# Optimization experiments

Hardware: AMD Instinct MI355X
Metric: run time of the kernel (lower is better)

Reference implementation:

```python
import jax, jax.numpy as jnp
import numpy as np

D_MODEL = 1024
NUM_HEADS = 16
D_K = D_MODEL // NUM_HEADS
D_MLP = 4096
EPS = 1e-5


def setup_inputs() -> dict:
    key = jax.random.key(0)
    ks = jax.random.split(key, 16)
    s = 0.02
    inp = {
        "x": jax.random.normal(ks[0], (2, 2048, D_MODEL), dtype=jnp.float32),
        "Wq": jax.random.normal(ks[1], (D_MODEL, D_MODEL), dtype=jnp.float32) * s,
        "bq": jnp.zeros((D_MODEL,), jnp.float32),
        "Wk": jax.random.normal(ks[2], (D_MODEL, D_MODEL), dtype=jnp.float32) * s,
        "bk": jnp.zeros((D_MODEL,), jnp.float32),
        "Wv": jax.random.normal(ks[3], (D_MODEL, D_MODEL), dtype=jnp.float32) * s,
        "bv": jnp.zeros((D_MODEL,), jnp.float32),
        "Wo": jax.random.normal(ks[4], (D_MODEL, D_MODEL), dtype=jnp.float32) * s,
        "bo": jnp.zeros((D_MODEL,), jnp.float32),
        "W1": jax.random.normal(ks[5], (D_MODEL, D_MLP), dtype=jnp.float32) * s,
        "b1": jnp.zeros((D_MLP,), jnp.float32),
        "W2": jax.random.normal(ks[6], (D_MLP, D_MODEL), dtype=jnp.float32) * s,
        "b2": jnp.zeros((D_MODEL,), jnp.float32),
        "ln1_g": jnp.ones((D_MODEL,), jnp.float32),
        "ln1_b": jnp.zeros((D_MODEL,), jnp.float32),
        "ln2_g": jnp.ones((D_MODEL,), jnp.float32),
        "ln2_b": jnp.zeros((D_MODEL,), jnp.float32),
    }
    return inp


def _layer_norm(x, g, b):
    mu = jnp.mean(x, axis=-1, keepdims=True)
    var = jnp.var(x, axis=-1, keepdims=True)
    return (x - mu) * jax.lax.rsqrt(var + EPS) * g + b


def _split_heads(x):
    b, s, _ = x.shape
    return x.reshape(b, s, NUM_HEADS, D_K).transpose(0, 2, 1, 3)  # [b,h,s,dk]


def reference(x, Wq, bq, Wk, bk, Wv, bv, Wo, bo, W1, b1, W2, b2,
              ln1_g, ln1_b, ln2_g, ln2_b):
    b, s, _ = x.shape
    q = _split_heads(x @ Wq + bq)
    k = _split_heads(x @ Wk + bk)
    v = _split_heads(x @ Wv + bv)
    # [b,h,s,s] scores, scaled by sqrt(d_k) as in the original
    score = jnp.einsum("bhqd,bhkd->bhqk", q, k) / jnp.sqrt(jnp.float32(D_K))
    attn = jax.nn.softmax(score, axis=-1)
    out = jnp.einsum("bhqk,bhkd->bhqd", attn, v)
    out = out.transpose(0, 2, 1, 3).reshape(b, s, D_MODEL)
    out = out @ Wo + bo
    # residual + norm1 (dropout is identity in eval)
    x = _layer_norm(x + out, ln1_g, ln1_b)
    # feed-forward
    h = jax.nn.relu(x @ W1 + b1)
    ff = h @ W2 + b2
    x = _layer_norm(x + ff, ln2_g, ln2_b)
    return x
```

## Files before the change

kernel.cpp:

```cpp
#include <hip/hip_runtime.h>
#include <hip/hip_bf16.h>
#include <cstdint>

#define DEV __device__ __forceinline__

typedef __attribute__((ext_vector_type(8))) __bf16 bf16x8;
typedef __attribute__((ext_vector_type(4))) float f32x4;

DEV uint16_t f2b(float f) {
  __hip_bfloat16 h = __float2bfloat16(f);
  return *(uint16_t*)&h;
}
DEV uint32_t pkbf2(float a, float b) {
  return (uint32_t)f2b(a) | ((uint32_t)f2b(b) << 16);
}

DEV void gload_lds16(const void* g, void* l) {
  __builtin_amdgcn_global_load_lds(
      (const __attribute__((address_space(1))) void*)g,
      (__attribute__((address_space(3))) void*)l, 16, 0, 0);
}

DEV bf16x8 scale8(bf16x8 v, float sc) {
  union { bf16x8 b; uint16_t u[8]; } in, out;
  in.b = v;
#pragma unroll
  for (int i = 0; i < 8; i++) {
    float x = __uint_as_float(((uint32_t)in.u[i]) << 16);
    out.u[i] = f2b(x * sc);
  }
  return out.b;
}

__global__ __launch_bounds__(256) void cast_bf16_kernel(
    const float* __restrict__ src, uint16_t* __restrict__ dst, int n4) {
  int i = blockIdx.x * 256 + threadIdx.x;
  if (i < n4) {
    float4 v = ((const float4*)src)[i];
    uint2 r;
    r.x = pkbf2(v.x, v.y);
    r.y = pkbf2(v.z, v.w);
    ((uint2*)dst)[i] = r;
  }
}

__global__ __launch_bounds__(256) void transpose_w(
    const float* __restrict__ src, uint16_t* __restrict__ dst, int R, int C) {
  __shared__ float t[32][33];
  int c0 = blockIdx.x * 32, r0 = blockIdx.y * 32;
  int tx = threadIdx.x & 31, ty = threadIdx.x >> 5;
#pragma unroll
  for (int i = 0; i < 4; i++)
    t[ty + 8 * i][tx] = src[(size_t)(r0 + ty + 8 * i) * C + c0 + tx];
  __syncthreads();
#pragma unroll
  for (int i = 0; i < 4; i++)
    dst[(size_t)(c0 + ty + 8 * i) * R + r0 + tx] = f2b(t[tx][ty + 8 * i]);
}

__global__ __launch_bounds__(256) void transpose_w3(
    const float* __restrict__ s0, const float* __restrict__ s1,
    const float* __restrict__ s2, uint16_t* __restrict__ dst) {
  __shared__ float t[32][33];
  const float* src = blockIdx.z == 0 ? s0 : (blockIdx.z == 1 ? s1 : s2);
  uint16_t* d = dst + (size_t)blockIdx.z * 1024 * 1024;
  int c0 = blockIdx.x * 32, r0 = blockIdx.y * 32;
  int tx = threadIdx.x & 31, ty = threadIdx.x >> 5;
#pragma unroll
  for (int i = 0; i < 4; i++)
    t[ty + 8 * i][tx] = src[(size_t)(r0 + ty + 8 * i) * 1024 + c0 + tx];
  __syncthreads();
#pragma unroll
  for (int i = 0; i < 4; i++)
    d[(size_t)(c0 + ty + 8 * i) * 1024 + r0 + tx] = f2b(t[tx][ty + 8 * i]);
}

__global__ __launch_bounds__(256) void transpose_v(
    const uint16_t* __restrict__ qkv, uint16_t* __restrict__ Vt) {
  __shared__ uint16_t t[32][33];
  int bh = blockIdx.z, b = bh >> 4, h = bh & 15;
  int s0 = blockIdx.x * 32, d0 = blockIdx.y * 32;
  int tx = threadIdx.x & 31, ty = threadIdx.x >> 5;
#pragma unroll
  for (int i = 0; i < 4; i++)
    t[ty + 8 * i][tx] =
        qkv[(size_t)(b * 2048 + s0 + ty + 8 * i) * 3072 + 2048 + h * 64 + d0 + tx];
  __syncthreads();
#pragma unroll
  for (int i = 0; i < 4; i++)
    Vt[((size_t)bh * 64 + d0 + ty + 8 * i) * 2048 + s0 + tx] = t[tx][ty + 8 * i];
}

__global__ __launch_bounds__(256) void concat3(
    const float* __restrict__ a, const float* __restrict__ b,
    const float* __restrict__ c, float* __restrict__ o) {
  int i = blockIdx.x * 256 + threadIdx.x;
  o[i] = i < 1024 ? a[i] : (i < 2048 ? b[i - 1024] : c[i - 2048]);
}

template <int MODE, int NSPLIT, int BK>
__global__ __launch_bounds__(256) void gemm_bt(
    const uint16_t* __restrict__ A, const uint16_t* __restrict__ Bt,
    const float* __restrict__ bias, void* __restrict__ Cv, void* __restrict__ Cv2,
    int M, int N, int K, int nx) {
  __shared__ uint16_t As[2][128 * BK];
  __shared__ uint16_t Bs[2][128 * BK];
  int nwg = gridDim.x, bid = blockIdx.x;
  int cpx = nwg >> 3;
  int swzb = (bid & 7) * cpx + (bid >> 3);
  int ntile = nwg / NSPLIT;
  int sp = swzb / ntile, r = swzb % ntile;
  int n0 = (r % nx) * 128, m0 = (r / nx) * 128;
  int Klen = K / NSPLIT;
  int tid = threadIdx.x, w = tid >> 6, l = tid & 63;
  int wr = w >> 1, wc = w & 1;
  int lr = l & 15, lg = l >> 4, lk8 = lg * 8;
  f32x4 acc[4][4] = {};
  const uint16_t* Ab = A + (size_t)m0 * K + sp * Klen;
  const uint16_t* Bb = Bt + (size_t)n0 * K + sp * Klen;

  auto stage = [&](int buf, int k0) {
    if (BK == 32) {
#pragma unroll
      for (int i = 0; i < 2; i++) {
        int c = 2 * w + i;
        int rr = c * 16 + (l >> 2);
        gload_lds16(Ab + (size_t)rr * K + k0 + (l & 3) * 8, &As[buf][c * 512]);
        gload_lds16(Bb + (size_t)rr * K + k0 + (l & 3) * 8, &Bs[buf][c * 512]);
      }
    } else {
      int colb = (((l & 7) ^ ((l >> 3) & 7)) << 4);
#pragma unroll
      for (int i = 0; i < 4; i++) {
        int c = 4 * w + i;
        int rr = c * 8 + (l >> 3);
        gload_lds16((const uint8_t*)(Ab + (size_t)rr * K + k0) + colb,
                    &As[buf][c * 512]);
        gload_lds16((const uint8_t*)(Bb + (size_t)rr * K + k0) + colb,
                    &Bs[buf][c * 512]);
      }
    }
  };

  stage(0, 0);
  __syncthreads();

  for (int k0 = 0; k0 < Klen; k0 += BK) {
    int cur = (k0 / BK) & 1;
    if (k0 + BK < Klen) stage(cur ^ 1, k0 + BK);
    if (BK == 32) {
      bf16x8 af[4], bf[4];
#pragma unroll
      for (int m = 0; m < 4; m++)
        af[m] = *(const bf16x8*)&As[cur][(wr * 64 + m * 16 + lr) * 32 + lk8];
#pragma unroll
      for (int n = 0; n < 4; n++)
        bf[n] = *(const bf16x8*)&Bs[cur][(wc * 64 + n * 16 + lr) * 32 + lk8];
#pragma unroll
      for (int m = 0; m < 4; m++)
#pragma unroll
        for (int n = 0; n < 4; n++)
          acc[m][n] = __builtin_amdgcn_mfma_f32_16x16x32_bf16(af[m], bf[n], acc[m][n], 0, 0, 0);
    } else {
      int sw = (lr & 7) << 4;
#pragma unroll
      for (int ks = 0; ks < 2; ks++) {
        int off = ((ks << 6) | (lg << 4)) ^ sw;
        bf16x8 af[4], bf[4];
#pragma unroll
        for (int m = 0; m < 4; m++)
          af[m] = *(const bf16x8*)((const uint8_t*)&As[cur][(wr * 64 + m * 16 + lr) * 64] + off);
#pragma unroll
        for (int n = 0; n < 4; n++)
          bf[n] = *(const bf16x8*)((const uint8_t*)&Bs[cur][(wc * 64 + n * 16 + lr) * 64] + off);
#pragma unroll
        for (int m = 0; m < 4; m++)
#pragma unroll
          for (int n = 0; n < 4; n++)
            acc[m][n] = __builtin_amdgcn_mfma_f32_16x16x32_bf16(af[m], bf[n], acc[m][n], 0, 0, 0);
      }
    }
    __syncthreads();
  }

  void* dstv = (NSPLIT == 1 || sp == 0) ? Cv : Cv2;
  int g4 = lg * 4;
#pragma unroll
  for (int m = 0; m < 4; m++) {
    int row = m0 + wr * 64 + m * 16 + g4;
#pragma unroll
    for (int n = 0; n < 4; n++) {
      int col = n0 + wc * 64 + n * 16 + lr;
      float bv = (NSPLIT == 1 || sp == 0) ? bias[col] : 0.f;
#pragma unroll
      for (int j = 0; j < 4; j++) {
        float v = acc[m][n][j] + bv;
        if (MODE == 2) v = fmaxf(v, 0.f);
        size_t idx = (size_t)(row + j) * N + col;
        if (MODE == 0) ((float*)dstv)[idx] = v;
        else           ((uint16_t*)dstv)[idx] = f2b(v);
      }
    }
  }
}

template <int MODE>
__global__ __launch_bounds__(512, 2) void gemm256(
    const uint16_t* __restrict__ A, const uint16_t* __restrict__ Bt,
    const float* __restrict__ bias, void* __restrict__ Cv,
    int M, int N, int K, int nx) {
  __shared__ uint16_t As[2][256 * 64];
  __shared__ uint16_t Bs[2][256 * 64];
  int nwg = gridDim.x, bid = blockIdx.x;
  int cpx = nwg >> 3;
  int swzb = (bid & 7) * cpx + (bid >> 3);
  int n0 = (swzb % nx) * 256, m0 = (swzb / nx) * 256;
  int tid = threadIdx.x, w = tid >> 6, l = tid & 63;
  int wr = w >> 2, wc = w & 3;
  int lr = l & 15, lg = l >> 4;
  f32x4 acc[8][4] = {};
  const uint16_t* Ab = A + (size_t)m0 * K;
  const uint16_t* Bb = Bt + (size_t)n0 * K;
  int colb = (((l & 7) ^ (l >> 3)) << 4);
  int srl = l >> 3;

  auto stageH = [&](int buf, int k0, int h) {
    const uint16_t* base = (h < 2) ? Ab : Bb;
    uint16_t* lds = (h < 2) ? &As[buf][0] : &Bs[buf][0];
    int hh = (h & 1) * 128;
#pragma unroll
    for (int j = 0; j < 2; j++) {
      int rr = hh + j * 64 + w * 8;
      gload_lds16((const uint8_t*)(base + (size_t)(rr + srl) * K + k0) + colb,
                  &lds[rr * 64]);
    }
  };

#pragma unroll
  for (int h = 0; h < 4; h++) stageH(0, 0, h);
  asm volatile("s_waitcnt vmcnt(0)" ::: "memory");
  __builtin_amdgcn_s_barrier();

  int nt = K >> 6;
  int swr = (lr & 7) << 4;
  for (int t = 0; t < nt; t++) {
    int buf = t & 1;
    bf16x8 bfr[2][4];
#pragma unroll
    for (int ks = 0; ks < 2; ks++) {
#pragma unroll
      for (int mq = 0; mq < 2; mq++) {
        const int ph = ks * 2 + mq;
        int off = ((ks << 6) | (lg << 4)) ^ swr;
        bf16x8 af[4];
#pragma unroll
        for (int m = 0; m < 4; m++) {
          int row = wr * 128 + (mq * 4 + m) * 16 + lr;
          af[m] = *(const bf16x8*)((const uint8_t*)&As[buf][row * 64] + off);
        }
        if (mq == 0) {
#pragma unroll
          for (int n = 0; n < 4; n++) {
            int row = wc * 64 + n * 16 + lr;
            bfr[ks][n] = *(const bf16x8*)((const uint8_t*)&Bs[buf][row * 64] + off);
          }
        }
        if (t + 1 < nt) {
          if (ph == 0) { stageH(buf ^ 1, (t + 1) * 64, 0); stageH(buf ^ 1, (t + 1) * 64, 1); }
          if (ph == 1) { stageH(buf ^ 1, (t + 1) * 64, 2); stageH(buf ^ 1, (t + 1) * 64, 3); }
        }
        __builtin_amdgcn_s_barrier();
        asm volatile("s_waitcnt lgkmcnt(0)" ::: "memory");
        __builtin_amdgcn_sched_barrier(0);
        __builtin_amdgcn_s_setprio(1);
#pragma unroll
        for (int m = 0; m < 4; m++)
#pragma unroll
          for (int n = 0; n < 4; n++)
            acc[mq * 4 + m][n] = __builtin_amdgcn_mfma_f32_16x16x32_bf16(
                af[m], bfr[ks][n], acc[mq * 4 + m][n], 0, 0, 0);
        __builtin_amdgcn_s_setprio(0);
        if (ph == 3) asm volatile("s_waitcnt vmcnt(0)" ::: "memory");
        __builtin_amdgcn_s_barrier();
      }
    }
  }

#pragma unroll
  for (int m = 0; m < 8; m++) {
    int row = m0 + wr * 128 + m * 16 + lg * 4;
#pragma unroll
    for (int n = 0; n < 4; n++) {
      int col = n0 + wc * 64 + n * 16 + lr;
      float bv = bias[col];
#pragma unroll
      for (int j = 0; j < 4; j++) {
        float v = acc[m][n][j] + bv;
        if (MODE == 2) v = fmaxf(v, 0.f);
        size_t idx = (size_t)(row + j) * N + col;
        if (MODE == 0) ((float*)Cv)[idx] = v;
        else           ((uint16_t*)Cv)[idx] = f2b(v);
      }
    }
  }
}

__global__ __launch_bounds__(256, 2) void attn_fused(
    const uint16_t* __restrict__ qkv, const uint16_t* __restrict__ Vt,
    uint16_t* __restrict__ outb) {
  constexpr int LQ = 3072;
  constexpr float SC = 0.18033688f;
  int L = blockIdx.x;
  int qb = (L >> 3) & 15;
  int bh = (L & 7) + 8 * (L >> 7);
  int b = bh >> 4, h = bh & 15;
  int w = threadIdx.x >> 6, l = threadIdx.x & 63;
  int lr = l & 15, lg = l >> 4;
  int qbase = qb * 128 + w * 32;

  __shared__ uint16_t Kbuf[2][2][64 * 64];
  __shared__ uint16_t Vbuf[2][2][64 * 64];
  __shared__ uint16_t Plds[4][2][16 * 64];
  uint16_t* PwA = &Plds[w][0][0];
  uint16_t* PwB = &Plds[w][1][0];

  const uint16_t* qrowA = qkv + (size_t)(b * 2048 + qbase + lr) * LQ + h * 64;
  const uint16_t* qrowB = qrowA + (size_t)16 * LQ;
  bf16x8 qA0 = scale8(*(const bf16x8*)(qrowA + lg * 8), SC);
  bf16x8 qA1 = scale8(*(const bf16x8*)(qrowA + 32 + lg * 8), SC);
  bf16x8 qB0 = scale8(*(const bf16x8*)(qrowB + lg * 8), SC);
  bf16x8 qB1 = scale8(*(const bf16x8*)(qrowB + 32 + lg * 8), SC);

  float rsA = 0.f, rsB = 0.f;
  f32x4 oA[4] = {}, oB[4] = {};

  const uint8_t* kq = (const uint8_t*)qkv;
  const uint8_t* vq = (const uint8_t*)Vt;
  int colb = (((l & 7) ^ ((l >> 3) & 7)) << 4);
  int Rl = w * 16 + (l >> 3);

  auto stageKV = [&](int buf, int kb) {
#pragma unroll
    for (int s2 = 0; s2 < 2; s2++) {
#pragma unroll
      for (int c2 = 0; c2 < 2; c2++) {
        int R = Rl + c2 * 8;
        const uint8_t* ks =
            kq + ((size_t)(b * 2048 + kb + s2 * 64 + R) * LQ + 1024 + h * 64) * 2 + colb;
        gload_lds16(ks, &Kbuf[buf][s2][(w * 16 + c2 * 8) * 64]);
        const uint8_t* vs =
            vq + ((size_t)(bh * 64 + R) * 2048 + kb + s2 * 64) * 2 + colb;
        gload_lds16(vs, &Vbuf[buf][s2][(w * 16 + c2 * 8) * 64]);
      }
    }
  };

  stageKV(0, 0);
  __syncthreads();

  int swz = (lr & 7) << 4;
  for (int kb = 0; kb < 2048; kb += 128) {
    int cur = (kb >> 7) & 1;
    if (kb + 128 < 2048) stageKV(cur ^ 1, kb + 128);

#pragma unroll
    for (int s2 = 0; s2 < 2; s2++) {
      const uint8_t* Kb = (const uint8_t*)Kbuf[cur][s2];
      const uint8_t* Vb = (const uint8_t*)Vbuf[cur][s2];
      f32x4 sA[4], sB[4];
      __builtin_amdgcn_s_setprio(1);
#pragma unroll
      for (int t = 0; t < 4; t++) {
        const uint8_t* rb = Kb + (16 * t + lr) * 128;
        bf16x8 k0 = *(const bf16x8*)(rb + ((lg << 4) ^ swz));
        bf16x8 k1 = *(const bf16x8*)(rb + ((64 | (lg << 4)) ^ swz));
        f32x4 zA = {};
        zA = __builtin_amdgcn_mfma_f32_16x16x32_bf16(k0, qA0, zA, 0, 0, 0);
        zA = __builtin_amdgcn_mfma_f32_16x16x32_bf16(k1, qA1, zA, 0, 0, 0);
        sA[t] = zA;
        f32x4 zB = {};
        zB = __builtin_amdgcn_mfma_f32_16x16x32_bf16(k0, qB0, zB, 0, 0, 0);
        zB = __builtin_amdgcn_mfma_f32_16x16x32_bf16(k1, qB1, zB, 0, 0, 0);
        sB[t] = zB;
      }
      __builtin_amdgcn_s_setprio(0);
#pragma unroll
      for (int t = 0; t < 4; t++) {
        float a0 = __builtin_amdgcn_exp2f(sA[t][0]);
        float a1 = __builtin_amdgcn_exp2f(sA[t][1]);
        float a2 = __builtin_amdgcn_exp2f(sA[t][2]);
        float a3 = __builtin_amdgcn_exp2f(sA[t][3]);
        rsA += (a0 + a1) + (a2 + a3);
        uint2 pa;
        pa.x = pkbf2(a0, a1);
        pa.y = pkbf2(a2, a3);
        *(uint2*)((uint8_t*)PwA + lr * 128 + ((t * 32 + lg * 8) ^ swz)) = pa;
        float b0 = __builtin_amdgcn_exp2f(sB[t][0]);
        float b1 = __builtin_amdgcn_exp2f(sB[t][1]);
        float b2 = __builtin_amdgcn_exp2f(sB[t][2]);
        float b3 = __builtin_amdgcn_exp2f(sB[t][3]);
        rsB += (b0 + b1) + (b2 + b3);
        uint2 pb;
        pb.x = pkbf2(b0, b1);
        pb.y = pkbf2(b2, b3);
        *(uint2*)((uint8_t*)PwB + lr * 128 + ((t * 32 + lg * 8) ^ swz)) = pb;
      }
      __builtin_amdgcn_wave_barrier();
      bf16x8 pA0 = *(const bf16x8*)((const uint8_t*)PwA + lr * 128 + ((lg << 4) ^ swz));
      bf16x8 pA1 = *(const bf16x8*)((const uint8_t*)PwA + lr * 128 + ((64 | (lg << 4)) ^ swz));
      bf16x8 pB0 = *(const bf16x8*)((const uint8_t*)PwB + lr * 128 + ((lg << 4) ^ swz));
      bf16x8 pB1 = *(const bf16x8*)((const uint8_t*)PwB + lr * 128 + ((64 | (lg << 4)) ^ swz));
      __builtin_amdgcn_s_setprio(1);
#pragma unroll
      for (int t = 0; t < 4; t++) {
        const uint8_t* rb = Vb + (16 * t + lr) * 128;
        bf16x8 v0 = *(const bf16x8*)(rb + ((lg << 4) ^ swz));
        bf16x8 v1 = *(const bf16x8*)(rb + ((64 | (lg << 4)) ^ swz));
        oA[t] = __builtin_amdgcn_mfma_f32_16x16x32_bf16(v0, pA0, oA[t], 0, 0, 0);
        oA[t] = __builtin_amdgcn_mfma_f32_16x16x32_bf16(v1, pA1, oA[t], 0, 0, 0);
        oB[t] = __builtin_amdgcn_mfma_f32_16x16x32_bf16(v0, pB0, oB[t], 0, 0, 0);
        oB[t] = __builtin_amdgcn_mfma_f32_16x16x32_bf16(v1, pB1, oB[t], 0, 0, 0);
      }
      __builtin_amdgcn_s_setprio(0);
      if (s2 == 0) __builtin_amdgcn_wave_barrier();
    }
    __syncthreads();
  }
  rsA += __shfl_xor(rsA, 16);
  rsA += __shfl_xor(rsA, 32);
  rsB += __shfl_xor(rsB, 16);
  rsB += __shfl_xor(rsB, 32);
  float invA = 1.f / rsA, invB = 1.f / rsB;
  uint16_t* orowA = outb + (size_t)(b * 2048 + qbase + lr) * 1024 + h * 64;
  uint16_t* orowB = orowA + (size_t)16 * 1024;
#pragma unroll
  for (int t = 0; t < 4; t++) {
    uint2 ra;
    ra.x = pkbf2(oA[t][0] * invA, oA[t][1] * invA);
    ra.y = pkbf2(oA[t][2] * invA, oA[t][3] * invA);
    *(uint2*)(orowA + t * 16 + lg * 4) = ra;
    uint2 rb2;
    rb2.x = pkbf2(oB[t][0] * invB, oB[t][1] * invB);
    rb2.y = pkbf2(oB[t][2] * invB, oB[t][3] * invB);
    *(uint2*)(orowB + t * 16 + lg * 4) = rb2;
  }
}

template <int XBF, int WF32, int WB16, int NR>
__global__ __launch_bounds__(256) void ln_res(
    const void* __restrict__ xr, const float* __restrict__ r0,
    const float* __restrict__ r1, const float* __restrict__ gam,
    const float* __restrict__ bet, float* __restrict__ of32,
    uint16_t* __restrict__ ob16) {
  int row = blockIdx.x, t = threadIdx.x;
  int w = t >> 6, l = t & 63;
  float v0, v1, v2, v3;
  if (XBF) {
    uint2 u = ((const uint2*)((const uint16_t*)xr + (size_t)row * 1024))[t];
    v0 = __uint_as_float((u.x & 0xffffu) << 16);
    v1 = __uint_as_float(u.x & 0xffff0000u);
    v2 = __uint_as_float((u.y & 0xffffu) << 16);
    v3 = __uint_as_float(u.y & 0xffff0000u);
  } else {
    float4 xv = ((const float4*)((const float*)xr + (size_t)row * 1024))[t];
    v0 = xv.x; v1 = xv.y; v2 = xv.z; v3 = xv.w;
  }
  float4 rv = ((const float4*)(r0 + (size_t)row * 1024))[t];
  v0 += rv.x; v1 += rv.y; v2 += rv.z; v3 += rv.w;
  if (NR == 2) {
    float4 r2 = ((const float4*)(r1 + (size_t)row * 1024))[t];
    v0 += r2.x; v1 += r2.y; v2 += r2.z; v3 += r2.w;
  }
  float s = v0 + v1 + v2 + v3;
  float sq = v0 * v0 + v1 * v1 + v2 * v2 + v3 * v3;
#pragma unroll
  for (int d = 1; d < 64; d <<= 1) {
    s += __shfl_xor(s, d);
    sq += __shfl_xor(sq, d);
  }
  __shared__ float red[8];
  if (l == 0) { red[w] = s; red[4 + w] = sq; }
  __syncthreads();
  s = red[0] + red[1] + red[2] + red[3];
  sq = red[4] + red[5] + red[6] + red[7];
  float mean = s * (1.f / 1024.f);
  float var = sq * (1.f / 1024.f) - mean * mean;
  float rstd = rsqrtf(var + 1e-5f);
  float4 gv = ((const float4*)gam)[t];
  float4 bv = ((const float4*)bet)[t];
  float y0 = (v0 - mean) * rstd * gv.x + bv.x;
  float y1 = (v1 - mean) * rstd * gv.y + bv.y;
  float y2 = (v2 - mean) * rstd * gv.z + bv.z;
  float y3 = (v3 - mean) * rstd * gv.w + bv.w;
  if (WF32) {
    float4 yv; yv.x = y0; yv.y = y1; yv.z = y2; yv.w = y3;
    ((float4*)(of32 + (size_t)row * 1024))[t] = yv;
  }
  if (WB16) {
    uint2 r;
    r.x = pkbf2(y0, y1);
    r.y = pkbf2(y2, y3);
    ((uint2*)(ob16 + (size_t)row * 1024))[t] = r;
  }
}

static constexpr size_t OFF_XB    = 0;
static constexpr size_t OFF_WQKVT = (size_t)8 << 20;
static constexpr size_t OFF_WOT   = (size_t)14 << 20;
static constexpr size_t OFF_W1T   = (size_t)16 << 20;
static constexpr size_t OFF_W2T   = (size_t)24 << 20;
static constexpr size_t OFF_BIAS  = (size_t)32 << 20;
static constexpr size_t OFF_QKV   = OFF_BIAS + ((size_t)64 << 10);
static constexpr size_t OFF_VT    = OFF_QKV + ((size_t)24 << 20);
static constexpr size_t OFF_PROJ  = OFF_VT + ((size_t)8 << 20);
static constexpr size_t OFF_LN1B  = OFF_PROJ + ((size_t)16 << 20);
static constexpr size_t OFF_PROJ2 = OFF_LN1B + ((size_t)8 << 20);

extern "C" void kernel_launch(void* const* d_in, const int* in_sizes, int n_in,
                              void* d_out, int out_size, void* d_ws, size_t ws_size,
                              hipStream_t stream) {
  const float* x   = (const float*)d_in[0];
  const float* Wq  = (const float*)d_in[1];
  const float* bq  = (const float*)d_in[2];
  const float* Wk  = (const float*)d_in[3];
  const float* bk  = (const float*)d_in[4];
  const float* Wv  = (const float*)d_in[5];
  const float* bv  = (const float*)d_in[6];
  const float* Wo  = (const float*)d_in[7];
  const float* bo  = (const float*)d_in[8];
  const float* W1  = (const float*)d_in[9];
  const float* b1  = (const float*)d_in[10];
  const float* W2  = (const float*)d_in[11];
  const float* b2  = (const float*)d_in[12];
  const float* g1  = (const float*)d_in[13];
  const float* be1 = (const float*)d_in[14];
  const float* g2  = (const float*)d_in[15];
  const float* be2 = (const float*)d_in[16];
  float* out = (float*)d_out;
  uint8_t* ws = (uint8_t*)d_ws;

  uint16_t* xb    = (uint16_t*)(ws + OFF_XB);
  uint16_t* wqkt  = (uint16_t*)(ws + OFF_WQKVT);
  uint16_t* wot   = (uint16_t*)(ws + OFF_WOT);
  uint16_t* w1t   = (uint16_t*)(ws + OFF_W1T);
  uint16_t* w2t   = (uint16_t*)(ws + OFF_W2T);
  float*    bqkv  = (float*)(ws + OFF_BIAS);
  uint16_t* qkvb  = (uint16_t*)(ws + OFF_QKV);
  uint16_t* vt    = (uint16_t*)(ws + OFF_VT);
  float*    proj  = (float*)(ws + OFF_PROJ);
  float*    proj2 = (float*)(ws + OFF_PROJ2);
  uint16_t* ln1b  = (uint16_t*)(ws + OFF_LN1B);
  uint16_t* attnb = (uint16_t*)(ws + OFF_XB);
  uint16_t* hbuf  = (uint16_t*)(ws + OFF_QKV);

  cast_bf16_kernel<<<4096, 256, 0, stream>>>(x, xb, 4096 * 1024 / 4);
  transpose_w3<<<dim3(32, 32, 3), 256, 0, stream>>>(Wq, Wk, Wv, wqkt);
  transpose_w<<<dim3(32, 32), 256, 0, stream>>>(Wo, wot, 1024, 1024);
  transpose_w<<<dim3(128, 32), 256, 0, stream>>>(W1, w1t, 1024, 4096);
  transpose_w<<<dim3(32, 128), 256, 0, stream>>>(W2, w2t, 4096, 1024);
  concat3<<<12, 256, 0, stream>>>(bq, bk, bv, bqkv);
  gemm_bt<1, 1, 32><<<768, 256, 0, stream>>>(xb, wqkt, bqkv, qkvb, nullptr,
                                             4096, 3072, 1024, 24);
  transpose_v<<<dim3(64, 2, 32), 256, 0, stream>>>(qkvb, vt);
  attn_fused<<<512, 256, 0, stream>>>(qkvb, vt, attnb);
  gemm_bt<0, 2, 64><<<512, 256, 0, stream>>>(attnb, wot, bo, proj, proj2,
                                             4096, 1024, 1024, 8);
  ln_res<0, 0, 1, 2><<<4096, 256, 0, stream>>>(x, proj, proj2, g1, be1,
                                               nullptr, ln1b);
  gemm256<2><<<256, 512, 0, stream>>>(ln1b, w1t, b1, hbuf, 4096, 4096, 1024, 16);
  gemm_bt<0, 2, 64><<<512, 256, 0, stream>>>(hbuf, w2t, b2, proj, proj2,
                                             4096, 1024, 4096, 8);
  ln_res<1, 1, 0, 2><<<4096, 256, 0, stream>>>(ln1b, proj, proj2, g2, be2,
                                               out, nullptr);
}
```

Measured before the change: 221.6 us.

## Switch attention to 32x32x16 MFMA with register shuffles instead of LDS for P

Rewrites the fused attention inner loop to use 32x32x16 bf16 MFMA tiles instead of 16x16x32. The probability matrix now moves from the score-accumulator layout to the B-operand layout through cross-lane shuffles rather than a round trip through per-wave LDS, and the Plds buffer and wave barriers are removed. This is meant to cut LDS traffic and MFMA issue count, at the cost of more register pressure and shuffle instructions. It also changes a template parameter of the QKV GEMM from 32 to 64.

```diff
diff --git a/kernel.cpp b/kernel.cpp
--- a/kernel.cpp
+++ b/kernel.cpp
@@ -6,6 +6,7 @@
 
 typedef __attribute__((ext_vector_type(8))) __bf16 bf16x8;
 typedef __attribute__((ext_vector_type(4))) float f32x4;
+typedef __attribute__((ext_vector_type(16))) float f32x16;
 
 DEV uint16_t f2b(float f) {
   __hip_bfloat16 h = __float2bfloat16(f);
@@ -315,24 +316,20 @@
   int bh = (L & 7) + 8 * (L >> 7);
   int b = bh >> 4, h = bh & 15;
   int w = threadIdx.x >> 6, l = threadIdx.x & 63;
-  int lr = l & 15, lg = l >> 4;
+  int l31 = l & 31, lh = l >> 5;
   int qbase = qb * 128 + w * 32;
 
   __shared__ uint16_t Kbuf[2][2][64 * 64];
   __shared__ uint16_t Vbuf[2][2][64 * 64];
-  __shared__ uint16_t Plds[4][2][16 * 64];
-  uint16_t* PwA = &Plds[w][0][0];
-  uint16_t* PwB = &Plds[w][1][0];
-
-  const uint16_t* qrowA = qkv + (size_t)(b * 2048 + qbase + lr) * LQ + h * 64;
-  const uint16_t* qrowB = qrowA + (size_t)16 * LQ;
-  bf16x8 qA0 = scale8(*(const bf16x8*)(qrowA + lg * 8), SC);
-  bf16x8 qA1 = scale8(*(const bf16x8*)(qrowA + 32 + lg * 8), SC);
-  bf16x8 qB0 = scale8(*(const bf16x8*)(qrowB + lg * 8), SC);
-  bf16x8 qB1 = scale8(*(const bf16x8*)(qrowB + 32 + lg * 8), SC);
-
-  float rsA = 0.f, rsB = 0.f;
-  f32x4 oA[4] = {}, oB[4] = {};
+
+  const uint16_t* qrow = qkv + (size_t)(b * 2048 + qbase + l31) * LQ + h * 64;
+  bf16x8 qf[4];
+#pragma unroll
+  for (int j = 0; j < 4; j++)
+    qf[j] = scale8(*(const bf16x8*)(qrow + j * 16 + lh * 8), SC);
+
+  float rs = 0.f;
+  f32x16 acc0 = {}, acc1 = {};
 
   const uint8_t* kq = (const uint8_t*)qkv;
   const uint8_t* vq = (const uint8_t*)Vt;
@@ -358,91 +355,79 @@
   stageKV(0, 0);
   __syncthreads();
 
-  int swz = (lr & 7) << 4;
+  bool lo = (lh == 0);
   for (int kb = 0; kb < 2048; kb += 128) {
     int cur = (kb >> 7) & 1;
     if (kb + 128 < 2048) stageKV(cur ^ 1, kb + 128);
 
 #pragma unroll
-    for (int s2 = 0; s2 < 2; s2++) {
+    for (int t32 = 0; t32 < 4; t32++) {
+      int s2 = t32 >> 1;
+      int ko = (t32 & 1) * 32;
       const uint8_t* Kb = (const uint8_t*)Kbuf[cur][s2];
       const uint8_t* Vb = (const uint8_t*)Vbuf[cur][s2];
-      f32x4 sA[4], sB[4];
+      int krow = ko + l31;
+      const uint8_t* krb = Kb + krow * 128;
+      int ksw = (krow & 7) << 4;
+      f32x16 s = {};
       __builtin_amdgcn_s_setprio(1);
 #pragma unroll
-      for (int t = 0; t < 4; t++) {
-        const uint8_t* rb = Kb + (16 * t + lr) * 128;
-        bf16x8 k0 = *(const bf16x8*)(rb + ((lg << 4) ^ swz));
-        bf16x8 k1 = *(const bf16x8*)(rb + ((64 | (lg << 4)) ^ swz));
-        f32x4 zA = {};
-        zA = __builtin_amdgcn_mfma_f32_16x16x32_bf16(k0, qA0, zA, 0, 0, 0);
-        zA = __builtin_amdgcn_mfma_f32_16x16x32_bf16(k1, qA1, zA, 0, 0, 0);
-        sA[t] = zA;
-        f32x4 zB = {};
-        zB = __builtin_amdgcn_mfma_f32_16x16x32_bf16(k0, qB0, zB, 0, 0, 0);
-        zB = __builtin_amdgcn_mfma_f32_16x16x32_bf16(k1, qB1, zB, 0, 0, 0);
-        sB[t] = zB;
+      for (int j = 0; j < 4; j++) {
+        bf16x8 kf = *(const bf16x8*)(krb + ((j * 32 + lh * 16) ^ ksw));
+        s = __builtin_amdgcn_mfma_f32_32x32x16_bf16(kf, qf[j], s, 0, 0, 0);
       }
       __builtin_amdgcn_s_setprio(0);
-#pragma unroll
-      for (int t = 0; t < 4; t++) {
-        float a0 = __builtin_amdgcn_exp2f(sA[t][0]);
-        float a1 = __builtin_amdgcn_exp2f(sA[t][1]);
-        float a2 = __builtin_amdgcn_exp2f(sA[t][2]);
-        float a3 = __builtin_amdgcn_exp2f(sA[t][3]);
-        rsA += (a0 + a1) + (a2 + a3);
-        uint2 pa;
-        pa.x = pkbf2(a0, a1);
-        pa.y = pkbf2(a2, a3);
-        *(uint2*)((uint8_t*)PwA + lr * 128 + ((t * 32 + lg * 8) ^ swz)) = pa;
-        float b0 = __builtin_amdgcn_exp2f(sB[t][0]);
-        float b1 = __builtin_amdgcn_exp2f(sB[t][1]);
-        float b2 = __builtin_amdgcn_exp2f(sB[t][2]);
-        float b3 = __builtin_amdgcn_exp2f(sB[t][3]);
-        rsB += (b0 + b1) + (b2 + b3);
-        uint2 pb;
-        pb.x = pkbf2(b0, b1);
-        pb.y = pkbf2(b2, b3);
-        *(uint2*)((uint8_t*)PwB + lr * 128 + ((t * 32 + lg * 8) ^ swz)) = pb;
-      }
-      __builtin_amdgcn_wave_barrier();
-      bf16x8 pA0 = *(const bf16x8*)((const uint8_t*)PwA + lr * 128 + ((lg << 4) ^ swz));
-      bf16x8 pA1 = *(const bf16x8*)((const uint8_t*)PwA + lr * 128 + ((64 | (lg << 4)) ^ swz));
-      bf16x8 pB0 = *(const bf16x8*)((const uint8_t*)PwB + lr * 128 + ((lg << 4) ^ swz));
-      bf16x8 pB1 = *(const bf16x8*)((const uint8_t*)PwB + lr * 128 + ((64 | (lg << 4)) ^ swz));
+      float p[16];
+#pragma unroll
+      for (int r = 0; r < 16; r++) p[r] = __builtin_amdgcn_exp2f(s[r]);
+#pragma unroll
+      for (int r = 0; r < 16; r += 4) rs += (p[r] + p[r + 1]) + (p[r + 2] + p[r + 3]);
+      uint32_t wv[8], sv[8];
+#pragma unroll
+      for (int i = 0; i < 8; i++) wv[i] = pkbf2(p[2 * i], p[2 * i + 1]);
+#pragma unroll
+      for (int i = 0; i < 8; i++) sv[i] = __shfl_xor(wv[i], 32);
+      union { uint32_t u[4]; bf16x8 v; } B1, B2;
+      B1.u[0] = lo ? wv[0] : sv[2];
+      B1.u[1] = lo ? wv[1] : sv[3];
+      B1.u[2] = lo ? sv[0] : wv[2];
+      B1.u[3] = lo ? sv[1] : wv[3];
+      B2.u[0] = lo ? wv[4] : sv[6];
+      B2.u[1] = lo ? wv[5] : sv[7];
+      B2.u[2] = lo ? sv[4] : wv[6];
+      B2.u[3] = lo ? sv[5] : wv[7];
+      int vsw = (l31 & 7) << 4;
+      const uint8_t* vrb0 = Vb + l31 * 128;
+      const uint8_t* vrb1 = Vb + (32 + l31) * 128;
       __builtin_amdgcn_s_setprio(1);
-#pragma unroll
-      for (int t = 0; t < 4; t++) {
-        const uint8_t* rb = Vb + (16 * t + lr) * 128;
-        bf16x8 v0 = *(const bf16x8*)(rb + ((lg << 4) ^ swz));
-        bf16x8 v1 = *(const bf16x8*)(rb + ((64 | (lg << 4)) ^ swz));
-        oA[t] = __builtin_amdgcn_mfma_f32_16x16x32_bf16(v0, pA0, oA[t], 0, 0, 0);
-        oA[t] = __builtin_amdgcn_mfma_f32_16x16x32_bf16(v1, pA1, oA[t], 0, 0, 0);
-        oB[t] = __builtin_amdgcn_mfma_f32_16x16x32_bf16(v0, pB0, oB[t], 0, 0, 0);
-        oB[t] = __builtin_amdgcn_mfma_f32_16x16x32_bf16(v1, pB1, oB[t], 0, 0, 0);
+      {
+        bf16x8 v00 = *(const bf16x8*)(vrb0 + ((ko * 2 + lh * 16) ^ vsw));
+        bf16x8 v01 = *(const bf16x8*)(vrb0 + ((ko * 2 + 32 + lh * 16) ^ vsw));
+        acc0 = __builtin_amdgcn_mfma_f32_32x32x16_bf16(v00, B1.v, acc0, 0, 0, 0);
+        acc0 = __builtin_amdgcn_mfma_f32_32x32x16_bf16(v01, B2.v, acc0, 0, 0, 0);
+        bf16x8 v10 = *(const bf16x8*)(vrb1 + ((ko * 2 + lh * 16) ^ vsw));
+        bf16x8 v11 = *(const bf16x8*)(vrb1 + ((ko * 2 + 32 + lh * 16) ^ vsw));
+        acc1 = __builtin_amdgcn_mfma_f32_32x32x16_bf16(v10, B1.v, acc1, 0, 0, 0);
+        acc1 = __builtin_amdgcn_mfma_f32_32x32x16_bf16(v11, B2.v, acc1, 0, 0, 0);
       }
       __builtin_amdgcn_s_setprio(0);
-      if (s2 == 0) __builtin_amdgcn_wave_barrier();
     }
     __syncthreads();
   }
-  rsA += __shfl_xor(rsA, 16);
-  rsA += __shfl_xor(rsA, 32);
-  rsB += __shfl_xor(rsB, 16);
-  rsB += __shfl_xor(rsB, 32);
-  float invA = 1.f / rsA, invB = 1.f / rsB;
-  uint16_t* orowA = outb + (size_t)(b * 2048 + qbase + lr) * 1024 + h * 64;
-  uint16_t* orowB = orowA + (size_t)16 * 1024;
-#pragma unroll
-  for (int t = 0; t < 4; t++) {
-    uint2 ra;
-    ra.x = pkbf2(oA[t][0] * invA, oA[t][1] * invA);
-    ra.y = pkbf2(oA[t][2] * invA, oA[t][3] * invA);
-    *(uint2*)(orowA + t * 16 + lg * 4) = ra;
-    uint2 rb2;
-    rb2.x = pkbf2(oB[t][0] * invB, oB[t][1] * invB);
-    rb2.y = pkbf2(oB[t][2] * invB, oB[t][3] * invB);
-    *(uint2*)(orowB + t * 16 + lg * 4) = rb2;
+  rs += __shfl_xor(rs, 32);
+  float inv = 1.f / rs;
+  uint16_t* orow = outb + (size_t)(b * 2048 + qbase + l31) * 1024 + h * 64;
+#pragma unroll
+  for (int dblk = 0; dblk < 2; dblk++) {
+    const f32x16& a = dblk ? acc1 : acc0;
+#pragma unroll
+    for (int g = 0; g < 4; g++) {
+      int d0 = dblk * 32 + g * 8 + 4 * lh;
+      uint2 r;
+      r.x = pkbf2(a[4 * g] * inv, a[4 * g + 1] * inv);
+      r.y = pkbf2(a[4 * g + 2] * inv, a[4 * g + 3] * inv);
+      *(uint2*)(orow + d0) = r;
+    }
   }
 }
 
@@ -559,7 +544,7 @@
   transpose_w<<<dim3(128, 32), 256, 0, stream>>>(W1, w1t, 1024, 4096);
   transpose_w<<<dim3(32, 128), 256, 0, stream>>>(W2, w2t, 4096, 1024);
   concat3<<<12, 256, 0, stream>>>(bq, bk, bv, bqkv);
-  gemm_bt<1, 1, 32><<<768, 256, 0, stream>>>(xb, wqkt, bqkv, qkvb, nullptr,
+  gemm_bt<1, 1, 64><<<768, 256, 0, stream>>>(xb, wqkt, bqkv, qkvb, nullptr,
                                              4096, 3072, 1024, 24);
   transpose_v<<<dim3(64, 2, 32), 256, 0, stream>>>(qkvb, vt);
   attn_fused<<<512, 256, 0, stream>>>(qkvb, vt, attnb);
```

Result: slower. 238.2 us (+7.5%).

## Merge prep kernels, store split-K partials in bf16, use gemm256 split-K for W2

Applied to the files above, without the earlier changes.

Six preprocessing launches (x cast, weight transposes, bias concat) become one prep_all kernel dispatched by block index. Split-K partial outputs for the Wo and W2 projections are now written as bf16 into one contiguous buffer, and ln_res sums a variable number of partials. The W2 GEMM moves from the 128-tile gemm_bt with 2 splits to the 256-tile gemm256 with 4 splits. The aim is less launch overhead, less partial-sum traffic and better tile reuse for the largest-K GEMM, at the cost of extra rounding from storing partials in bf16.

```diff
diff --git a/kernel.cpp b/kernel.cpp
--- a/kernel.cpp
+++ b/kernel.cpp
@@ -32,23 +32,55 @@
   return out.b;
 }
 
-__global__ __launch_bounds__(256) void cast_bf16_kernel(
-    const float* __restrict__ src, uint16_t* __restrict__ dst, int n4) {
-  int i = blockIdx.x * 256 + threadIdx.x;
-  if (i < n4) {
-    float4 v = ((const float4*)src)[i];
+__global__ __launch_bounds__(256) void prep_all(
+    const float* __restrict__ x, uint16_t* __restrict__ xb,
+    const float* __restrict__ Wq, const float* __restrict__ Wk,
+    const float* __restrict__ Wv, uint16_t* __restrict__ wqkt,
+    const float* __restrict__ Wo, uint16_t* __restrict__ wot,
+    const float* __restrict__ W1, uint16_t* __restrict__ w1t,
+    const float* __restrict__ W2, uint16_t* __restrict__ w2t,
+    const float* __restrict__ bq, const float* __restrict__ bk,
+    const float* __restrict__ bv, float* __restrict__ bqkv) {
+  __shared__ float t[32][33];
+  int bid = blockIdx.x, tid = threadIdx.x;
+  if (bid < 4096) {
+    int i = bid * 256 + tid;
+    float4 v = ((const float4*)x)[i];
     uint2 r;
     r.x = pkbf2(v.x, v.y);
     r.y = pkbf2(v.z, v.w);
-    ((uint2*)dst)[i] = r;
-  }
-}
-
-__global__ __launch_bounds__(256) void transpose_w(
-    const float* __restrict__ src, uint16_t* __restrict__ dst, int R, int C) {
-  __shared__ float t[32][33];
-  int c0 = blockIdx.x * 32, r0 = blockIdx.y * 32;
-  int tx = threadIdx.x & 31, ty = threadIdx.x >> 5;
+    ((uint2*)xb)[i] = r;
+    return;
+  }
+  if (bid >= 16384) {
+    int i = (bid - 16384) * 256 + tid;
+    if (i < 3072)
+      bqkv[i] = i < 1024 ? bq[i] : (i < 2048 ? bk[i - 1024] : bv[i - 2048]);
+    return;
+  }
+  const float* src;
+  uint16_t* dst;
+  int R, C, bx, by;
+  if (bid < 8192) {
+    int local = bid - 4096;
+    if (local < 3072) {
+      int z = local >> 10, rem = local & 1023;
+      src = z == 0 ? Wq : (z == 1 ? Wk : Wv);
+      dst = wqkt + (size_t)z * 1024 * 1024;
+      R = 1024; C = 1024; bx = rem & 31; by = rem >> 5;
+    } else {
+      int rem = local - 3072;
+      src = Wo; dst = wot; R = 1024; C = 1024; bx = rem & 31; by = rem >> 5;
+    }
+  } else if (bid < 12288) {
+    int rem = bid - 8192;
+    src = W1; dst = w1t; R = 1024; C = 4096; bx = rem & 127; by = rem >> 7;
+  } else {
+    int rem = bid - 12288;
+    src = W2; dst = w2t; R = 4096; C = 1024; bx = rem & 31; by = rem >> 5;
+  }
+  int c0 = bx * 32, r0 = by * 32;
+  int tx = tid & 31, ty = tid >> 5;
 #pragma unroll
   for (int i = 0; i < 4; i++)
     t[ty + 8 * i][tx] = src[(size_t)(r0 + ty + 8 * i) * C + c0 + tx];
@@ -56,23 +88,6 @@
 #pragma unroll
   for (int i = 0; i < 4; i++)
     dst[(size_t)(c0 + ty + 8 * i) * R + r0 + tx] = f2b(t[tx][ty + 8 * i]);
-}
-
-__global__ __launch_bounds__(256) void transpose_w3(
-    const float* __restrict__ s0, const float* __restrict__ s1,
-    const float* __restrict__ s2, uint16_t* __restrict__ dst) {
-  __shared__ float t[32][33];
-  const float* src = blockIdx.z == 0 ? s0 : (blockIdx.z == 1 ? s1 : s2);
-  uint16_t* d = dst + (size_t)blockIdx.z * 1024 * 1024;
-  int c0 = blockIdx.x * 32, r0 = blockIdx.y * 32;
-  int tx = threadIdx.x & 31, ty = threadIdx.x >> 5;
-#pragma unroll
-  for (int i = 0; i < 4; i++)
-    t[ty + 8 * i][tx] = src[(size_t)(r0 + ty + 8 * i) * 1024 + c0 + tx];
-  __syncthreads();
-#pragma unroll
-  for (int i = 0; i < 4; i++)
-    d[(size_t)(c0 + ty + 8 * i) * 1024 + r0 + tx] = f2b(t[tx][ty + 8 * i]);
 }
 
 __global__ __launch_bounds__(256) void transpose_v(
@@ -91,17 +106,10 @@
     Vt[((size_t)bh * 64 + d0 + ty + 8 * i) * 2048 + s0 + tx] = t[tx][ty + 8 * i];
 }
 
-__global__ __launch_bounds__(256) void concat3(
-    const float* __restrict__ a, const float* __restrict__ b,
-    const float* __restrict__ c, float* __restrict__ o) {
-  int i = blockIdx.x * 256 + threadIdx.x;
-  o[i] = i < 1024 ? a[i] : (i < 2048 ? b[i - 1024] : c[i - 2048]);
-}
-
 template <int MODE, int NSPLIT, int BK>
 __global__ __launch_bounds__(256) void gemm_bt(
     const uint16_t* __restrict__ A, const uint16_t* __restrict__ Bt,
-    const float* __restrict__ bias, void* __restrict__ Cv, void* __restrict__ Cv2,
+    const float* __restrict__ bias, void* __restrict__ Cv,
     int M, int N, int K, int nx) {
   __shared__ uint16_t As[2][128 * BK];
   __shared__ uint16_t Bs[2][128 * BK];
@@ -183,7 +191,6 @@
     __syncthreads();
   }
 
-  void* dstv = (NSPLIT == 1 || sp == 0) ? Cv : Cv2;
   int g4 = lg * 4;
 #pragma unroll
   for (int m = 0; m < 4; m++) {
@@ -196,15 +203,15 @@
       for (int j = 0; j < 4; j++) {
         float v = acc[m][n][j] + bv;
         if (MODE == 2) v = fmaxf(v, 0.f);
-        size_t idx = (size_t)(row + j) * N + col;
-        if (MODE == 0) ((float*)dstv)[idx] = v;
-        else           ((uint16_t*)dstv)[idx] = f2b(v);
-      }
-    }
-  }
-}
-
-template <int MODE>
+        size_t idx = (size_t)sp * M * N + (size_t)(row + j) * N + col;
+        if (MODE == 0) ((float*)Cv)[idx] = v;
+        else           ((uint16_t*)Cv)[idx] = f2b(v);
+      }
+    }
+  }
+}
+
+template <int MODE, int NSPLIT>
 __global__ __launch_bounds__(512, 2) void gemm256(
     const uint16_t* __restrict__ A, const uint16_t* __restrict__ Bt,
     const float* __restrict__ bias, void* __restrict__ Cv,
@@ -214,13 +221,16 @@
   int nwg = gridDim.x, bid = blockIdx.x;
   int cpx = nwg >> 3;
   int swzb = (bid & 7) * cpx + (bid >> 3);
-  int n0 = (swzb % nx) * 256, m0 = (swzb / nx) * 256;
+  int ntile = nwg / NSPLIT;
+  int sp = swzb / ntile, rr0 = swzb % ntile;
+  int n0 = (rr0 % nx) * 256, m0 = (rr0 / nx) * 256;
+  int Klen = K / NSPLIT;
   int tid = threadIdx.x, w = tid >> 6, l = tid & 63;
   int wr = w >> 2, wc = w & 3;
   int lr = l & 15, lg = l >> 4;
   f32x4 acc[8][4] = {};
-  const uint16_t* Ab = A + (size_t)m0 * K;
-  const uint16_t* Bb = Bt + (size_t)n0 * K;
+  const uint16_t* Ab = A + (size_t)m0 * K + sp * Klen;
+  const uint16_t* Bb = Bt + (size_t)n0 * K + sp * Klen;
   int colb = (((l & 7) ^ (l >> 3)) << 4);
   int srl = l >> 3;
 
@@ -241,7 +251,7 @@
   asm volatile("s_waitcnt vmcnt(0)" ::: "memory");
   __builtin_amdgcn_s_barrier();
 
-  int nt = K >> 6;
+  int nt = Klen >> 6;
   int swr = (lr & 7) << 4;
   for (int t = 0; t < nt; t++) {
     int buf = t & 1;
@@ -292,12 +302,12 @@
 #pragma unroll
     for (int n = 0; n < 4; n++) {
       int col = n0 + wc * 64 + n * 16 + lr;
-      float bv = bias[col];
+      float bv = (NSPLIT == 1 || sp == 0) ? bias[col] : 0.f;
 #pragma unroll
       for (int j = 0; j < 4; j++) {
         float v = acc[m][n][j] + bv;
         if (MODE == 2) v = fmaxf(v, 0.f);
-        size_t idx = (size_t)(row + j) * N + col;
+        size_t idx = (size_t)sp * M * N + (size_t)(row + j) * N + col;
         if (MODE == 0) ((float*)Cv)[idx] = v;
         else           ((uint16_t*)Cv)[idx] = f2b(v);
       }
@@ -446,12 +456,11 @@
   }
 }
 
-template <int XBF, int WF32, int WB16, int NR>
+template <int XBF, int WF32, int WB16, int NPART>
 __global__ __launch_bounds__(256) void ln_res(
-    const void* __restrict__ xr, const float* __restrict__ r0,
-    const float* __restrict__ r1, const float* __restrict__ gam,
-    const float* __restrict__ bet, float* __restrict__ of32,
-    uint16_t* __restrict__ ob16) {
+    const void* __restrict__ xr, const uint16_t* __restrict__ parts,
+    const float* __restrict__ gam, const float* __restrict__ bet,
+    float* __restrict__ of32, uint16_t* __restrict__ ob16) {
   int row = blockIdx.x, t = threadIdx.x;
   int w = t >> 6, l = t & 63;
   float v0, v1, v2, v3;
@@ -465,11 +474,14 @@
     float4 xv = ((const float4*)((const float*)xr + (size_t)row * 1024))[t];
     v0 = xv.x; v1 = xv.y; v2 = xv.z; v3 = xv.w;
   }
-  float4 rv = ((const float4*)(r0 + (size_t)row * 1024))[t];
-  v0 += rv.x; v1 += rv.y; v2 += rv.z; v3 += rv.w;
-  if (NR == 2) {
-    float4 r2 = ((const float4*)(r1 + (size_t)row * 1024))[t];
-    v0 += r2.x; v1 += r2.y; v2 += r2.z; v3 += r2.w;
+#pragma unroll
+  for (int p = 0; p < NPART; p++) {
+    uint2 u = ((const uint2*)(parts + (size_t)p * 4096 * 1024 +
+                              (size_t)row * 1024))[t];
+    v0 += __uint_as_float((u.x & 0xffffu) << 16);
+    v1 += __uint_as_float(u.x & 0xffff0000u);
+    v2 += __uint_as_float((u.y & 0xffffu) << 16);
+    v3 += __uint_as_float(u.y & 0xffff0000u);
   }
   float s = v0 + v1 + v2 + v3;
   float sq = v0 * v0 + v1 * v1 + v2 * v2 + v3 * v3;
@@ -513,8 +525,7 @@
 static constexpr size_t OFF_QKV   = OFF_BIAS + ((size_t)64 << 10);
 static constexpr size_t OFF_VT    = OFF_QKV + ((size_t)24 << 20);
 static constexpr size_t OFF_PROJ  = OFF_VT + ((size_t)8 << 20);
-static constexpr size_t OFF_LN1B  = OFF_PROJ + ((size_t)16 << 20);
-static constexpr size_t OFF_PROJ2 = OFF_LN1B + ((size_t)8 << 20);
+static constexpr size_t OFF_LN1B  = OFF_PROJ + ((size_t)32 << 20);
 
 extern "C" void kernel_launch(void* const* d_in, const int* in_sizes, int n_in,
                               void* d_out, int out_size, void* d_ws, size_t ws_size,
@@ -547,29 +558,25 @@
   float*    bqkv  = (float*)(ws + OFF_BIAS);
   uint16_t* qkvb  = (uint16_t*)(ws + OFF_QKV);
   uint16_t* vt    = (uint16_t*)(ws + OFF_VT);
-  float*    proj  = (float*)(ws + OFF_PROJ);
-  float*    proj2 = (float*)(ws + OFF_PROJ2);
+  uint16_t* proj  = (uint16_t*)(ws + OFF_PROJ);
   uint16_t* ln1b  = (uint16_t*)(ws + OFF_LN1B);
   uint16_t* attnb = (uint16_t*)(ws + OFF_XB);
   uint16_t* hbuf  = (uint16_t*)(ws + OFF_QKV);
 
-  cast_bf16_kernel<<<4096, 256, 0, stream>>>(x, xb, 4096 * 1024 / 4);
-  transpose_w3<<<dim3(32, 32, 3), 256, 0, stream>>>(Wq, Wk, Wv, wqkt);
-  transpose_w<<<dim3(32, 32), 256, 0, stream>>>(Wo, wot, 1024, 1024);
-  transpose_w<<<dim3(128, 32), 256, 0, stream>>>(W1, w1t, 1024, 4096);
-  transpose_w<<<dim3(32, 128), 256, 0, stream>>>(W2, w2t, 4096, 1024);
-  concat3<<<12, 256, 0, stream>>>(bq, bk, bv, bqkv);
-  gemm_bt<1, 1, 32><<<768, 256, 0, stream>>>(xb, wqkt, bqkv, qkvb, nullptr,
+  prep_all<<<16396, 256, 0, stream>>>(x, xb, Wq, Wk, Wv, wqkt, Wo, wot,
+                                      W1, w1t, W2, w2t, bq, bk, bv, bqkv);
+  gemm_bt<1, 1, 32><<<768, 256, 0, stream>>>(xb, wqkt, bqkv, qkvb,
                                              4096, 3072, 1024, 24);
   transpose_v<<<dim3(64, 2, 32), 256, 0, stream>>>(qkvb, vt);
   attn_fused<<<512, 256, 0, stream>>>(qkvb, vt, attnb);
-  gemm_bt<0, 2, 64><<<512, 256, 0, stream>>>(attnb, wot, bo, proj, proj2,
+  gemm_bt<1, 2, 64><<<512, 256, 0, stream>>>(attnb, wot, bo, proj,
                                              4096, 1024, 1024, 8);
-  ln_res<0, 0, 1, 2><<<4096, 256, 0, stream>>>(x, proj, proj2, g1, be1,
+  ln_res<0, 0, 1, 2><<<4096, 256, 0, stream>>>(x, proj, g1, be1,
                                                nullptr, ln1b);
-  gemm256<2><<<256, 512, 0, stream>>>(ln1b, w1t, b1, hbuf, 4096, 4096, 1024, 16);
-  gemm_bt<0, 2, 64><<<512, 256, 0, stream>>>(hbuf, w2t, b2, proj, proj2,
-                                             4096, 1024, 4096, 8);
-  ln_res<1, 1, 0, 2><<<4096, 256, 0, stream>>>(ln1b, proj, proj2, g2, be2,
+  gemm256<2, 1><<<256, 512, 0, stream>>>(ln1b, w1t, b1, hbuf,
+                                         4096, 4096, 1024, 16);
+  gemm256<1, 4><<<256, 512, 0, stream>>>(hbuf, w2t, b2, proj,
+                                         4096, 1024, 4096, 4);
+  ln_res<1, 1, 0, 4><<<4096, 256, 0, stream>>>(ln1b, proj, g2, be2,
                                                out, nullptr);
 }
```

Result: faster. 211.1 us (-4.8%).
